# Performance work log

Measured on AMD Instinct MI355X. Metric: run time of the kernel, lower is better.

## Reference

```python
import jax, jax.numpy as jnp
import numpy as np

NUM_NODES = 100000
NUM_EDGES = 1200000
IN_CH = 64
HID_CH = 64
NUM_REL = 8
DEG = NUM_EDGES // NUM_NODES  # uniform degree 12


def setup_inputs() -> dict:
    key = jax.random.key(0)
    k1, k2, k3, k4 = jax.random.split(key, 4)
    x = jax.random.normal(k1, (NUM_NODES, IN_CH), dtype=jnp.float32)
    linear = jax.random.normal(k2, (NUM_REL, IN_CH, HID_CH), dtype=jnp.float32) * (1.0 / np.sqrt(IN_CH))
    ptr = jnp.arange(NUM_NODES + 1, dtype=jnp.int64) * DEG  # CSR row pointers, uniform degree
    idx = jax.random.randint(k3, (NUM_EDGES,), 0, NUM_NODES, dtype=jnp.int64)
    edge_types = jax.random.randint(k4, (NUM_EDGES,), 0, NUM_REL, dtype=jnp.int64)
    return {"x": x, "linear": linear, "ptr": ptr, "idx": idx,
            "edge_types": edge_types, "num_node": NUM_NODES}


def reference(x, linear, ptr, idx, edge_types, num_node):
    # Gather source-node features per edge: [E, in]
    gathered = x[idx]
    # Per-edge-type linear transform (loop over small fixed num_rel, like RGCNOP)
    out_e = jnp.zeros((gathered.shape[0], linear.shape[-1]), dtype=gathered.dtype)
    for r in range(linear.shape[0]):
        mask = (edge_types == r).astype(gathered.dtype)[:, None]
        out_e = out_e + mask * (gathered @ linear[r])
    # CSR scatter-sum aggregation over destination segments defined by ptr
    num_edges = idx.shape[0]
    seg_ids = jnp.searchsorted(ptr, jnp.arange(num_edges, dtype=ptr.dtype), side='right') - 1
    agg = jax.ops.segment_sum(out_e, seg_ids, num_segments=num_node)
    # Degree normalization
    deg = (ptr[1:] - ptr[:-1]).astype(agg.dtype)
    return agg / deg[:, None]
```

## Files before the change

kernel.cpp:

```cpp
#include <hip/hip_runtime.h>
#include <hip/hip_bf16.h>


#define THREADS 512
#define NPB 32
#define KDIM 512
#define LDA 520
#define MAXE 512
#define WFRAG (4 * 16 * 64 * 8)

typedef __attribute__((ext_vector_type(8))) short bf16x8;
typedef __attribute__((ext_vector_type(4))) float f32x4;

extern __shared__ __align__(16) char smem[];

__device__ __forceinline__ unsigned short f2bf(float f) {
  __hip_bfloat16 h = __float2bfloat16(f);
  return *reinterpret_cast<unsigned short*>(&h);
}

__global__ __launch_bounds__(256) void pack_w(const void* __restrict__ wv,
                                              unsigned short* __restrict__ wsB) {
  const int lane = threadIdx.x & 63;
  const unsigned word = ((const unsigned*)wv)[lane];
  const int exf = (int)((word >> 7) & 0xFFu);
  const bool w_bf16 = __popcll(__ballot(exf >= 96 && exf < 160)) >= 48;
  const int i = blockIdx.x * 256 + threadIdx.x;
  if (i < WFRAG) {
    const int j  = i & 7;
    const int l  = (i >> 3) & 63;
    const int kt = (i >> 9) & 15;
    const int nt = i >> 13;
    const int k  = kt * 32 + (l >> 4) * 8 + j;
    const int n  = nt * 16 + (l & 15);
    float v;
    if (w_bf16) v = __bfloat162float(((const __hip_bfloat16*)wv)[k * 64 + n]);
    else        v = ((const float*)wv)[k * 64 + n];
    wsB[i] = f2bf(v);
  }
}

#define ACC_SW(accrow, r, vv)                                        \
  switch (r) {                                                       \
    case 0: accrow[0] += (vv); break; case 1: accrow[1] += (vv); break; \
    case 2: accrow[2] += (vv); break; case 3: accrow[3] += (vv); break; \
    case 4: accrow[4] += (vv); break; case 5: accrow[5] += (vv); break; \
    case 6: accrow[6] += (vv); break; default: accrow[7] += (vv); break; }

__global__ __launch_bounds__(THREADS, 8)
void rgcn_fused(const void* __restrict__ xv,
                const void* __restrict__ wv,
                const int* __restrict__ p32,
                const int* __restrict__ i32,
                const int* __restrict__ t32,
                const unsigned short* __restrict__ wsB,
                float* __restrict__ out,
                int num_nodes) {
  __hip_bfloat16* aggS = (__hip_bfloat16*)smem;
  __hip_bfloat16* wtS  = aggS + NPB * LDA;
  char* tail = smem + (size_t)NPB * LDA * 2 + (wsB ? 0 : (size_t)64 * LDA * 2);
  float*    invS  = (float*)tail;
  int*      ptrS  = (int*)(tail + 256);
  unsigned* eMeta = (unsigned*)(tail + 256 + 272);

  const int tid   = threadIdx.x;
  const int lane  = tid & 63;
  const int wvid  = tid >> 6;
  const int node0 = blockIdx.x * NPB;

  const unsigned xword = ((const unsigned*)xv)[lane];
  const int exf = (int)((xword >> 7) & 0xFFu);
  const bool x_bf16 = __popcll(__ballot(exf >= 96 && exf < 160)) >= 48;
  const bool idx64 = (p32[1] == 0);

  auto ldptr = [&](int n) -> int { return idx64 ? p32[2 * n] : p32[n]; };

  const int ntop   = min(node0 + NPB, num_nodes);
  const int e_lo   = ldptr(node0);
  const int ecount = ldptr(ntop) - e_lo;
  const bool staged = (ecount > 0 && ecount <= MAXE);

  for (int i = tid; i <= NPB; i += THREADS)
    ptrS[i] = ldptr(min(node0 + i, num_nodes));

  if (staged) {
    for (int e = tid; e < ecount; e += THREADS) {
      const int ge = e_lo + e;
      const unsigned s = (unsigned)(idx64 ? i32[2 * ge] : i32[ge]);
      const unsigned r = (unsigned)(idx64 ? t32[2 * ge] : t32[ge]);
      eMeta[e] = s | (r << 24);
    }
  }

  if (!wsB) {
    if (x_bf16) {
      const __hip_bfloat16* wb = (const __hip_bfloat16*)wv;
      for (int i = tid; i < KDIM * 64; i += THREADS)
        wtS[(i & 63) * LDA + (i >> 6)] = wb[i];
    } else {
      const float* wf = (const float*)wv;
      for (int i = tid; i < KDIM * 64; i += THREADS)
        wtS[(i & 63) * LDA + (i >> 6)] = __float2bfloat16(wf[i]);
    }
  }

  __syncthreads();

  for (int i = tid; i < NPB; i += THREADS) {
    const int d = ptrS[i + 1] - ptrS[i];
    invS[i] = (d > 0 && node0 + i < num_nodes) ? 1.0f / (float)d : 0.0f;
  }

  if (staged && tid < NPB) {
    const int e0 = ptrS[tid] - e_lo;
    if (ptrS[tid + 1] - ptrS[tid] == 12) {
      unsigned a[12];
#pragma unroll
      for (int j = 0; j < 12; ++j) a[j] = eMeta[e0 + j];
#pragma unroll
      for (int r = 0; r < 12; ++r)
#pragma unroll
        for (int i = (r & 1); i + 1 < 12; i += 2) {
          const unsigned lo = min(a[i], a[i + 1]);
          const unsigned hi = max(a[i], a[i + 1]);
          a[i] = lo; a[i + 1] = hi;
        }
#pragma unroll
      for (int j = 0; j < 12; ++j) eMeta[e0 + j] = a[j];
    }
  }

  __syncthreads();

  const int c16 = lane & 15;
  const int qd  = lane >> 4;

  auto gather = [&](auto loadrow) {
    const int nlb = wvid * 4;
    const int eq0 = ptrS[nlb + qd] - e_lo;
    const int dq  = ptrS[nlb + qd + 1] - e_lo - eq0;
    const bool okfast = staged && (node0 + nlb + 3 < num_nodes) &&
                        (__ballot(dq == 12) == ~0ull);
    if (okfast) {
      unsigned m[12];
#pragma unroll
      for (int j = 0; j < 12; ++j) m[j] = eMeta[eq0 + j];

      unsigned short* dst0 =
          (unsigned short*)(aggS + (nlb + qd) * LDA) + 4 * c16;
      const ushort4 z4 = {0, 0, 0, 0};
#pragma unroll
      for (int r = 0; r < 8; ++r) *(ushort4*)(dst0 + r * 64) = z4;

      float4 cur = make_float4(0.f, 0.f, 0.f, 0.f);
      unsigned prev = 0xFFFFFFFFu;
#pragma unroll
      for (int b = 0; b < 2; ++b) {
        float4 v[6];
#pragma unroll
        for (int j = 0; j < 6; ++j)
          v[j] = loadrow((int)(m[b * 6 + j] & 0x00FFFFFFu), c16);
        __builtin_amdgcn_sched_barrier(0);
#pragma unroll
        for (int j = 0; j < 6; ++j) {
          const unsigned rj = m[b * 6 + j] >> 24;
          const float mk = (rj == prev) ? 1.0f : 0.0f;
          cur.x = fmaf(cur.x, mk, v[j].x);
          cur.y = fmaf(cur.y, mk, v[j].y);
          cur.z = fmaf(cur.z, mk, v[j].z);
          cur.w = fmaf(cur.w, mk, v[j].w);
          ushort4 bb;
          bb.x = f2bf(cur.x); bb.y = f2bf(cur.y);
          bb.z = f2bf(cur.z); bb.w = f2bf(cur.w);
          *(ushort4*)(dst0 + rj * 64) = bb;
          prev = rj;
        }
      }
    } else {
#pragma unroll
      for (int t = 0; t < 4; ++t) {
        const int nl = nlb + t;
        float a[8] = {0.f, 0.f, 0.f, 0.f, 0.f, 0.f, 0.f, 0.f};
        if (node0 + nl < num_nodes) {
          const int e0 = ptrS[nl] - e_lo, e1 = ptrS[nl + 1] - e_lo;
          for (int e = e0; e < e1; ++e) {
            unsigned mm;
            if (staged) mm = eMeta[e];
            else {
              const int ge = e_lo + e;
              mm = (unsigned)(idx64 ? i32[2 * ge] : i32[ge]) |
                   ((unsigned)(idx64 ? t32[2 * ge] : t32[ge]) << 24);
            }
            const size_t off = (size_t)(mm & 0x00FFFFFFu) * 64 + lane;
            const float vv = x_bf16
                ? __bfloat162float(((const __hip_bfloat16*)xv)[off])
                : ((const float*)xv)[off];
            const int r = __builtin_amdgcn_readfirstlane((int)(mm >> 24));
            ACC_SW(a, r, vv)
          }
        }
#pragma unroll
        for (int r = 0; r < 8; ++r)
          aggS[nl * LDA + r * 64 + lane] = __float2bfloat16(a[r]);
      }
    }
  };

  if (x_bf16) {
    auto lr = [&](int src, int c) -> float4 {
      const ushort4 u = ((const ushort4*)xv)[src * 16 + c];
      float4 f;
      f.x = __uint_as_float((unsigned)(unsigned short)u.x << 16);
      f.y = __uint_as_float((unsigned)(unsigned short)u.y << 16);
      f.z = __uint_as_float((unsigned)(unsigned short)u.z << 16);
      f.w = __uint_as_float((unsigned)(unsigned short)u.w << 16);
      return f;
    };
    gather(lr);
  } else {
    auto lr = [&](int src, int c) -> float4 {
      return ((const float4*)xv)[src * 16 + c];
    };
    gather(lr);
  }

  __syncthreads();

  const int mt = wvid >> 2;
  const int nt = wvid & 3;
  const int mi = lane & 15;
  const int q4 = lane >> 4;
  const __hip_bfloat16* ap = aggS + (mt * 16 + mi) * LDA + q4 * 8;
  f32x4 c0 = {0.f, 0.f, 0.f, 0.f};
  if (wsB) {
    const bf16x8* B = (const bf16x8*)wsB;
#pragma unroll
    for (int kt = 0; kt < KDIM / 32; ++kt) {
      const bf16x8 a = *(const bf16x8*)(ap + kt * 32);
      const bf16x8 b = B[(nt * 16 + kt) * 64 + lane];
      c0 = __builtin_amdgcn_mfma_f32_16x16x32_bf16(a, b, c0, 0, 0, 0);
    }
  } else {
    const __hip_bfloat16* bp = wtS + (nt * 16 + mi) * LDA + q4 * 8;
#pragma unroll
    for (int kt = 0; kt < KDIM / 32; ++kt) {
      const bf16x8 a = *(const bf16x8*)(ap + kt * 32);
      const bf16x8 b = *(const bf16x8*)(bp + kt * 32);
      c0 = __builtin_amdgcn_mfma_f32_16x16x32_bf16(a, b, c0, 0, 0, 0);
    }
  }

#pragma unroll
  for (int i = 0; i < 4; ++i) {
    const int nl   = mt * 16 + q4 * 4 + i;
    const int node = node0 + nl;
    if (node < num_nodes)
      out[(size_t)node * 64 + nt * 16 + mi] = c0[i] * invS[nl];
  }
}

extern "C" void kernel_launch(void* const* d_in, const int* in_sizes, int n_in,
                              void* d_out, int out_size, void* d_ws, size_t ws_size,
                              hipStream_t stream) {
  const void* x   = d_in[0];
  const void* w   = d_in[1];
  const int*  ptr = (const int*)d_in[2];
  const int*  idx = (const int*)d_in[3];
  const int*  et  = (const int*)d_in[4];
  float*      out = (float*)d_out;

  const int num_nodes = in_sizes[0] / 64;

  const bool haveB = (d_ws != nullptr) &&
                     (ws_size >= (size_t)WFRAG * sizeof(unsigned short));
  unsigned short* wsB = haveB ? (unsigned short*)d_ws : nullptr;
  if (haveB) pack_w<<<WFRAG / 256, 256, 0, stream>>>(w, wsB);

  const size_t lds_bytes = (size_t)NPB * LDA * 2 +
                           (haveB ? 0 : (size_t)64 * LDA * 2) +
                           256 + 272 + (size_t)MAXE * 4;

  hipFuncSetAttribute((const void*)rgcn_fused,
                      hipFuncAttributeMaxDynamicSharedMemorySize,
                      (int)lds_bytes);

  const int nblocks = (num_nodes + NPB - 1) / NPB;
  rgcn_fused<<<nblocks, THREADS, lds_bytes, stream>>>(x, w, ptr, idx, et, wsB,
                                                      out, num_nodes);
}
```

Before: 139.5 us.

## Pre-convert node features to bf16 in workspace and gather half-width rows

Adds a pack_x kernel that converts x to bf16 in the workspace each call. The fused kernel then gathers 8-byte bf16 rows instead of 16-byte fp32 rows in the fast path, and issues all 12 loads before accumulating. The aim is to halve random-gather traffic, at the cost of an extra full pass over x (read 25.6MB, write 12.8MB) plus a launch. The fallback path keeps the original fp32 loads with the loads also merged into one batch of 12.

```diff
diff --git a/kernel.cpp b/kernel.cpp
--- a/kernel.cpp
+++ b/kernel.cpp
@@ -40,6 +40,33 @@
   }
 }
 
+__global__ __launch_bounds__(256) void pack_x(const void* __restrict__ xv,
+                                              unsigned short* __restrict__ wsX,
+                                              int nx) {
+  const int lane = threadIdx.x & 63;
+  const unsigned word = ((const unsigned*)xv)[lane];
+  const int exf = (int)((word >> 7) & 0xFFu);
+  const bool x_bf16 = __popcll(__ballot(exf >= 96 && exf < 160)) >= 48;
+  const int base = (blockIdx.x * 256 + threadIdx.x) * 8;
+  if (base + 8 <= nx) {
+    if (x_bf16) {
+      *(uint4*)(wsX + base) = *(const uint4*)((const unsigned short*)xv + base);
+    } else {
+      const float4 a = *(const float4*)((const float*)xv + base);
+      const float4 b = *(const float4*)((const float*)xv + base + 4);
+      ushort4 lo, hi;
+      lo.x = f2bf(a.x); lo.y = f2bf(a.y); lo.z = f2bf(a.z); lo.w = f2bf(a.w);
+      hi.x = f2bf(b.x); hi.y = f2bf(b.y); hi.z = f2bf(b.z); hi.w = f2bf(b.w);
+      *(ushort4*)(wsX + base)     = lo;
+      *(ushort4*)(wsX + base + 4) = hi;
+    }
+  } else if (base < nx) {
+    for (int i = base; i < nx; ++i)
+      wsX[i] = x_bf16 ? ((const unsigned short*)xv)[i]
+                      : f2bf(((const float*)xv)[i]);
+  }
+}
+
 #define ACC_SW(accrow, r, vv)                                        \
   switch (r) {                                                       \
     case 0: accrow[0] += (vv); break; case 1: accrow[1] += (vv); break; \
@@ -54,6 +81,7 @@
                 const int* __restrict__ i32,
                 const int* __restrict__ t32,
                 const unsigned short* __restrict__ wsB,
+                const unsigned short* __restrict__ wsX,
                 float* __restrict__ out,
                 int num_nodes) {
   __hip_bfloat16* aggS = (__hip_bfloat16*)smem;
@@ -135,93 +163,118 @@
   const int c16 = lane & 15;
   const int qd  = lane >> 4;
 
-  auto gather = [&](auto loadrow) {
-    const int nlb = wvid * 4;
-    const int eq0 = ptrS[nlb + qd] - e_lo;
-    const int dq  = ptrS[nlb + qd + 1] - e_lo - eq0;
-    const bool okfast = staged && (node0 + nlb + 3 < num_nodes) &&
-                        (__ballot(dq == 12) == ~0ull);
-    if (okfast) {
-      unsigned m[12];
-#pragma unroll
-      for (int j = 0; j < 12; ++j) m[j] = eMeta[eq0 + j];
-
-      unsigned short* dst0 =
-          (unsigned short*)(aggS + (nlb + qd) * LDA) + 4 * c16;
-      const ushort4 z4 = {0, 0, 0, 0};
-#pragma unroll
-      for (int r = 0; r < 8; ++r) *(ushort4*)(dst0 + r * 64) = z4;
-
-      float4 cur = make_float4(0.f, 0.f, 0.f, 0.f);
-      unsigned prev = 0xFFFFFFFFu;
-#pragma unroll
-      for (int b = 0; b < 2; ++b) {
-        float4 v[6];
-#pragma unroll
-        for (int j = 0; j < 6; ++j)
-          v[j] = loadrow((int)(m[b * 6 + j] & 0x00FFFFFFu), c16);
-        __builtin_amdgcn_sched_barrier(0);
-#pragma unroll
-        for (int j = 0; j < 6; ++j) {
-          const unsigned rj = m[b * 6 + j] >> 24;
-          const float mk = (rj == prev) ? 1.0f : 0.0f;
-          cur.x = fmaf(cur.x, mk, v[j].x);
-          cur.y = fmaf(cur.y, mk, v[j].y);
-          cur.z = fmaf(cur.z, mk, v[j].z);
-          cur.w = fmaf(cur.w, mk, v[j].w);
-          ushort4 bb;
-          bb.x = f2bf(cur.x); bb.y = f2bf(cur.y);
-          bb.z = f2bf(cur.z); bb.w = f2bf(cur.w);
-          *(ushort4*)(dst0 + rj * 64) = bb;
-          prev = rj;
+  const int nlb = wvid * 4;
+  const int eq0 = ptrS[nlb + qd] - e_lo;
+  const int dq  = ptrS[nlb + qd + 1] - e_lo - eq0;
+  const bool okfast = staged && (node0 + nlb + 3 < num_nodes) &&
+                      (__ballot(dq == 12) == ~0ull);
+
+  if (okfast && wsX) {
+    unsigned m[12];
+#pragma unroll
+    for (int j = 0; j < 12; ++j) m[j] = eMeta[eq0 + j];
+
+    uint2 u[12];
+#pragma unroll
+    for (int j = 0; j < 12; ++j)
+      u[j] = ((const uint2*)wsX)[(size_t)(m[j] & 0x00FFFFFFu) * 16 + c16];
+    __builtin_amdgcn_sched_barrier(0);
+
+    unsigned short* dst0 = (unsigned short*)(aggS + (nlb + qd) * LDA) + 4 * c16;
+    const ushort4 z4 = {0, 0, 0, 0};
+#pragma unroll
+    for (int r = 0; r < 8; ++r) *(ushort4*)(dst0 + r * 64) = z4;
+
+    float4 cur = make_float4(0.f, 0.f, 0.f, 0.f);
+    unsigned prev = 0xFFFFFFFFu;
+#pragma unroll
+    for (int j = 0; j < 12; ++j) {
+      const unsigned rj = m[j] >> 24;
+      const float mk = (rj == prev) ? 1.0f : 0.0f;
+      const float vx = __uint_as_float(u[j].x << 16);
+      const float vy = __uint_as_float(u[j].x & 0xFFFF0000u);
+      const float vz = __uint_as_float(u[j].y << 16);
+      const float vw = __uint_as_float(u[j].y & 0xFFFF0000u);
+      cur.x = fmaf(cur.x, mk, vx);
+      cur.y = fmaf(cur.y, mk, vy);
+      cur.z = fmaf(cur.z, mk, vz);
+      cur.w = fmaf(cur.w, mk, vw);
+      ushort4 bb;
+      bb.x = f2bf(cur.x); bb.y = f2bf(cur.y);
+      bb.z = f2bf(cur.z); bb.w = f2bf(cur.w);
+      *(ushort4*)(dst0 + rj * 64) = bb;
+      prev = rj;
+    }
+  } else if (okfast) {
+    unsigned m[12];
+#pragma unroll
+    for (int j = 0; j < 12; ++j) m[j] = eMeta[eq0 + j];
+    float4 v[12];
+    if (x_bf16) {
+#pragma unroll
+      for (int j = 0; j < 12; ++j) {
+        const ushort4 us =
+            ((const ushort4*)xv)[(size_t)(m[j] & 0x00FFFFFFu) * 16 + c16];
+        v[j].x = __uint_as_float((unsigned)(unsigned short)us.x << 16);
+        v[j].y = __uint_as_float((unsigned)(unsigned short)us.y << 16);
+        v[j].z = __uint_as_float((unsigned)(unsigned short)us.z << 16);
+        v[j].w = __uint_as_float((unsigned)(unsigned short)us.w << 16);
+      }
+    } else {
+#pragma unroll
+      for (int j = 0; j < 12; ++j)
+        v[j] = ((const float4*)xv)[(size_t)(m[j] & 0x00FFFFFFu) * 16 + c16];
+    }
+    __builtin_amdgcn_sched_barrier(0);
+
+    unsigned short* dst0 = (unsigned short*)(aggS + (nlb + qd) * LDA) + 4 * c16;
+    const ushort4 z4 = {0, 0, 0, 0};
+#pragma unroll
+    for (int r = 0; r < 8; ++r) *(ushort4*)(dst0 + r * 64) = z4;
+
+    float4 cur = make_float4(0.f, 0.f, 0.f, 0.f);
+    unsigned prev = 0xFFFFFFFFu;
+#pragma unroll
+    for (int j = 0; j < 12; ++j) {
+      const unsigned rj = m[j] >> 24;
+      const float mk = (rj == prev) ? 1.0f : 0.0f;
+      cur.x = fmaf(cur.x, mk, v[j].x);
+      cur.y = fmaf(cur.y, mk, v[j].y);
+      cur.z = fmaf(cur.z, mk, v[j].z);
+      cur.w = fmaf(cur.w, mk, v[j].w);
+      ushort4 bb;
+      bb.x = f2bf(cur.x); bb.y = f2bf(cur.y);
+      bb.z = f2bf(cur.z); bb.w = f2bf(cur.w);
+      *(ushort4*)(dst0 + rj * 64) = bb;
+      prev = rj;
+    }
+  } else {
+#pragma unroll
+    for (int t = 0; t < 4; ++t) {
+      const int nl = nlb + t;
+      float a[8] = {0.f, 0.f, 0.f, 0.f, 0.f, 0.f, 0.f, 0.f};
+      if (node0 + nl < num_nodes) {
+        const int e0 = ptrS[nl] - e_lo, e1 = ptrS[nl + 1] - e_lo;
+        for (int e = e0; e < e1; ++e) {
+          unsigned mm;
+          if (staged) mm = eMeta[e];
+          else {
+            const int ge = e_lo + e;
+            mm = (unsigned)(idx64 ? i32[2 * ge] : i32[ge]) |
+                 ((unsigned)(idx64 ? t32[2 * ge] : t32[ge]) << 24);
+          }
+          const size_t off = (size_t)(mm & 0x00FFFFFFu) * 64 + lane;
+          const float vv = x_bf16
+              ? __bfloat162float(((const __hip_bfloat16*)xv)[off])
+              : ((const float*)xv)[off];
+          const int r = __builtin_amdgcn_readfirstlane((int)(mm >> 24));
+          ACC_SW(a, r, vv)
         }
       }
-    } else {
-#pragma unroll
-      for (int t = 0; t < 4; ++t) {
-        const int nl = nlb + t;
-        float a[8] = {0.f, 0.f, 0.f, 0.f, 0.f, 0.f, 0.f, 0.f};
-        if (node0 + nl < num_nodes) {
-          const int e0 = ptrS[nl] - e_lo, e1 = ptrS[nl + 1] - e_lo;
-          for (int e = e0; e < e1; ++e) {
-            unsigned mm;
-            if (staged) mm = eMeta[e];
-            else {
-              const int ge = e_lo + e;
-              mm = (unsigned)(idx64 ? i32[2 * ge] : i32[ge]) |
-                   ((unsigned)(idx64 ? t32[2 * ge] : t32[ge]) << 24);
-            }
-            const size_t off = (size_t)(mm & 0x00FFFFFFu) * 64 + lane;
-            const float vv = x_bf16
-                ? __bfloat162float(((const __hip_bfloat16*)xv)[off])
-                : ((const float*)xv)[off];
-            const int r = __builtin_amdgcn_readfirstlane((int)(mm >> 24));
-            ACC_SW(a, r, vv)
-          }
-        }
-#pragma unroll
-        for (int r = 0; r < 8; ++r)
-          aggS[nl * LDA + r * 64 + lane] = __float2bfloat16(a[r]);
-      }
-    }
-  };
-
-  if (x_bf16) {
-    auto lr = [&](int src, int c) -> float4 {
-      const ushort4 u = ((const ushort4*)xv)[src * 16 + c];
-      float4 f;
-      f.x = __uint_as_float((unsigned)(unsigned short)u.x << 16);
-      f.y = __uint_as_float((unsigned)(unsigned short)u.y << 16);
-      f.z = __uint_as_float((unsigned)(unsigned short)u.z << 16);
-      f.w = __uint_as_float((unsigned)(unsigned short)u.w << 16);
-      return f;
-    };
-    gather(lr);
-  } else {
-    auto lr = [&](int src, int c) -> float4 {
-      return ((const float4*)xv)[src * 16 + c];
-    };
-    gather(lr);
+#pragma unroll
+      for (int r = 0; r < 8; ++r)
+        aggS[nl * LDA + r * 64 + lane] = __float2bfloat16(a[r]);
+    }
   }
 
   __syncthreads();
@@ -270,11 +323,20 @@
   float*      out = (float*)d_out;
 
   const int num_nodes = in_sizes[0] / 64;
-
-  const bool haveB = (d_ws != nullptr) &&
-                     (ws_size >= (size_t)WFRAG * sizeof(unsigned short));
+  const int nx = num_nodes * 64;
+
+  const size_t needB = (size_t)WFRAG * 2;
+  const size_t needX = needB + (size_t)nx * 2;
+  const bool haveB = (d_ws != nullptr) && (ws_size >= needB);
+  const bool haveX = (d_ws != nullptr) && (ws_size >= needX);
   unsigned short* wsB = haveB ? (unsigned short*)d_ws : nullptr;
+  unsigned short* wsX = haveX ? (unsigned short*)d_ws + WFRAG : nullptr;
+
   if (haveB) pack_w<<<WFRAG / 256, 256, 0, stream>>>(w, wsB);
+  if (haveX) {
+    const int nthreads = (nx + 7) / 8;
+    pack_x<<<(nthreads + 255) / 256, 256, 0, stream>>>(x, wsX, nx);
+  }
 
   const size_t lds_bytes = (size_t)NPB * LDA * 2 +
                            (haveB ? 0 : (size_t)64 * LDA * 2) +
@@ -286,5 +348,5 @@
 
   const int nblocks = (num_nodes + NPB - 1) / NPB;
   rgcn_fused<<<nblocks, THREADS, lds_bytes, stream>>>(x, w, ptr, idx, et, wsB,
-                                                      out, num_nodes);
-}
+                                                      wsX, out, num_nodes);
+}
```

New measurement: 137.8 us. No clear change (-1.2%).
